# Performance work log

Hardware: AMD Instinct MI355X
Metric: run time of the kernel (lower is better)

The kernel has to match this reference:

```python
import jax, jax.numpy as jnp
import numpy as np

D_MODEL = 1024
N_HEADS = 16
D_K = D_MODEL // N_HEADS
NEG_INF = -1.0e9


def setup_inputs() -> dict:
    key = jax.random.key(0)
    ks = jax.random.split(key, 12)
    B, S = 2, 2048
    inp = {
        "q": jax.random.normal(ks[0], (B, S, D_MODEL), dtype=jnp.float32),
        "k": jax.random.normal(ks[1], (B, S, D_MODEL), dtype=jnp.float32),
        "v": jax.random.normal(ks[2], (B, S, D_MODEL), dtype=jnp.float32),
        "mask": jax.random.randint(ks[3], (B, 1, S, S), 0, 2, dtype=jnp.int32),
        "Wq": jax.random.normal(ks[4], (D_MODEL, D_MODEL), dtype=jnp.float32) / np.sqrt(D_MODEL),
        "bq": jnp.zeros((D_MODEL,), dtype=jnp.float32),
        "Wk": jax.random.normal(ks[5], (D_MODEL, D_MODEL), dtype=jnp.float32) / np.sqrt(D_MODEL),
        "bk": jnp.zeros((D_MODEL,), dtype=jnp.float32),
        "Wv": jax.random.normal(ks[6], (D_MODEL, D_MODEL), dtype=jnp.float32) / np.sqrt(D_MODEL),
        "bv": jnp.zeros((D_MODEL,), dtype=jnp.float32),
        "Wo": jax.random.normal(ks[7], (D_MODEL, D_MODEL), dtype=jnp.float32) / np.sqrt(D_MODEL),
        "bo": jnp.zeros((D_MODEL,), dtype=jnp.float32),
    }
    return inp


def _split_heads(x):
    B, S, _ = x.shape
    return x.reshape(B, S, N_HEADS, D_K).transpose(0, 2, 1, 3)  # [B,H,S,Dk]


def reference(q, k, v, mask, Wq, bq, Wk, bk, Wv, bv, Wo, bo):
    # QKV projections (nn.Linear: x @ W.T + b; here W stored as [in,out]-agnostic square)
    query = _split_heads(q @ Wq + bq)
    key_ = _split_heads(k @ Wk + bk)
    value = _split_heads(v @ Wv + bv)

    scale = 1.0 / np.sqrt(D_K).astype(np.float32)
    scores = jnp.einsum("bhqd,bhkd->bhqk", query, key_) * scale  # [B,H,S,S]
    scores = jnp.where(mask == 0, NEG_INF, scores)
    attn = jax.nn.softmax(scores, axis=-1)  # dropout is identity in eval (p=0.0)
    ctx = jnp.einsum("bhqk,bhkd->bhqd", attn, value)  # [B,H,S,Dk]

    B, H, S, Dk = ctx.shape
    ctx = ctx.transpose(0, 2, 1, 3).reshape(B, S, H * Dk)
    return ctx @ Wo + bo
```

## Files before the change

### kernel.cpp

```cpp
#include <hip/hip_runtime.h>
#include <hip/hip_bf16.h>

typedef __bf16 bf16_t;
typedef __bf16 bf16x2 __attribute__((ext_vector_type(2)));
typedef __bf16 bf16x4 __attribute__((ext_vector_type(4)));
typedef __bf16 bf16x8 __attribute__((ext_vector_type(8)));
typedef float f32x4 __attribute__((ext_vector_type(4)));
typedef float f32x16 __attribute__((ext_vector_type(16)));
typedef int intx4 __attribute__((ext_vector_type(4)));
typedef unsigned int u32;
typedef unsigned long long u64;

#define S_LEN 2048
#define DM 1024
#define NH 16
#define DK 64
#define M_ROWS 4096
#define SCALE_LOG2E 0.1803368801111204f

__device__ __forceinline__ int sw_off(int row, int col) {
  return row * 64 + ((((col >> 3) ^ row) & 7) << 3) + (col & 7);
}

__device__ __forceinline__ bf16x8 cvt8(const float4& a, const float4& b) {
  bf16x8 v;
  v[0] = (__bf16)a.x; v[1] = (__bf16)a.y; v[2] = (__bf16)a.z; v[3] = (__bf16)a.w;
  v[4] = (__bf16)b.x; v[5] = (__bf16)b.y; v[6] = (__bf16)b.z; v[7] = (__bf16)b.w;
  return v;
}

__device__ __forceinline__ void glds16(const bf16_t* g, bf16_t* l) {
  __builtin_amdgcn_global_load_lds(
      (const __attribute__((address_space(1))) void*)g,
      (__attribute__((address_space(3))) void*)l, 16, 0, 0);
}

__device__ __forceinline__ int pk2(float lo, float hi) {
  bf16x2 t;
  t[0] = (__bf16)lo;
  t[1] = (__bf16)hi;
  return __builtin_bit_cast(int, t);
}

__global__ __launch_bounds__(256) void prep(
    const float* __restrict__ q, const float* __restrict__ k,
    const float* __restrict__ v, bf16_t* __restrict__ Xb,
    const float* __restrict__ Wq, const float* __restrict__ Wk,
    const float* __restrict__ Wv, const float* __restrict__ Wo,
    bf16_t* __restrict__ Wt,
    const int* __restrict__ mask, u64* __restrict__ mb)
{
  __shared__ float tile[64][65];
  const int blk = blockIdx.x;
  if (blk < 6144) {
    const int z = blk >> 11;
    const int bx = blk & 2047;
    const float* __restrict__ src = (z == 0) ? q : ((z == 1) ? k : v);
    const size_t idx = ((size_t)bx * 256 + threadIdx.x) * 8;
    const float4 a = *(const float4*)&src[idx];
    const float4 b = *(const float4*)&src[idx + 4];
    *(bf16x8*)&Xb[(size_t)z * M_ROWS * DM + idx] = cvt8(a, b);
  } else if (blk < 7168) {
    const int idx = blk - 6144;
    const int z = idx >> 8, by = (idx >> 4) & 15, bx = idx & 15;
    const float* __restrict__ W = (z == 0) ? Wq : ((z == 1) ? Wk : ((z == 2) ? Wv : Wo));
    bf16_t* __restrict__ out = Wt + (size_t)z * DM * DM;
    const int tx = threadIdx.x & 31, ty = threadIdx.x >> 5;
    const int k0 = bx * 64, n0 = by * 64;
    #pragma unroll
    for (int j = 0; j < 8; ++j) {
      const float2 vv = *(const float2*)&W[(size_t)(k0 + ty + 8 * j) * DM + n0 + tx * 2];
      tile[ty + 8 * j][tx * 2] = vv.x;
      tile[ty + 8 * j][tx * 2 + 1] = vv.y;
    }
    __syncthreads();
    #pragma unroll
    for (int j = 0; j < 8; ++j) {
      const int a = ty + 8 * j;
      bf16x2 p;
      p[0] = (__bf16)tile[tx * 2][a];
      p[1] = (__bf16)tile[tx * 2 + 1][a];
      *(bf16x2*)&out[(size_t)(n0 + a) * DM + k0 + tx * 2] = p;
    }
  } else {
    const int g = (blk - 7168) * 256 + threadIdx.x;
    const int qq = g & 2047;
    const int kw = (g >> 11) & 31;
    const int b = g >> 16;
    const int* src = &mask[((size_t)(b * S_LEN + qq)) * S_LEN + kw * 64];
    u64 bits = 0;
    #pragma unroll
    for (int i = 0; i < 16; ++i) {
      const int4 m4 = *(const int4*)&src[i * 4];
      bits |= (u64)(m4.x != 0) << (4 * i);
      bits |= (u64)(m4.y != 0) << (4 * i + 1);
      bits |= (u64)(m4.z != 0) << (4 * i + 2);
      bits |= (u64)(m4.w != 0) << (4 * i + 3);
    }
    mb[g] = bits;
  }
}

__device__ __forceinline__ void gemm128_body(
    const bf16_t* __restrict__ A, const bf16_t* __restrict__ Bt,
    const float* __restrict__ bias, const float scale,
    bf16_t* __restrict__ outb, float* __restrict__ outf,
    bf16_t* __restrict__ vtw)
{
  __shared__ __align__(16) bf16_t Smem[128 * 136];
  bf16_t* As = Smem;
  bf16_t* Bs = Smem + 4096;
  const int t = threadIdx.x, w = t >> 6, L = t & 63, quad = L >> 4, l16 = L & 15;
  const int m0 = blockIdx.x * 128, n0 = blockIdx.y * 128;
  const int mb = 64 * (w & 1), nb = 64 * (w >> 1);
  const int rowS = t >> 2, subS = (t & 3) * 8;

  f32x4 acc[4][4] = {};
  for (int k0 = 0; k0 < DM; k0 += 32) {
    __syncthreads();
    glds16(&A[(size_t)(m0 + rowS) * DM + k0 + subS],        &As[t * 8]);
    glds16(&A[(size_t)(m0 + 64 + rowS) * DM + k0 + subS],   &As[2048 + t * 8]);
    glds16(&Bt[(size_t)(n0 + rowS) * DM + k0 + subS],       &Bs[t * 8]);
    glds16(&Bt[(size_t)(n0 + 64 + rowS) * DM + k0 + subS],  &Bs[2048 + t * 8]);
    __syncthreads();
    bf16x8 af[4], bfr[4];
    #pragma unroll
    for (int mt = 0; mt < 4; ++mt)
      af[mt] = *(const bf16x8*)&As[(mb + 16 * mt + l16) * 32 + quad * 8];
    #pragma unroll
    for (int ct = 0; ct < 4; ++ct)
      bfr[ct] = *(const bf16x8*)&Bs[(nb + 16 * ct + l16) * 32 + quad * 8];
    #pragma unroll
    for (int mt = 0; mt < 4; ++mt)
      #pragma unroll
      for (int ct = 0; ct < 4; ++ct)
        acc[mt][ct] = __builtin_amdgcn_mfma_f32_16x16x32_bf16(af[mt], bfr[ct], acc[mt][ct], 0, 0, 0);
  }

  if (vtw) {
    __syncthreads();
    #pragma unroll
    for (int mt = 0; mt < 4; ++mt)
      #pragma unroll
      for (int ct = 0; ct < 4; ++ct) {
        const int nloc = nb + 16 * ct + l16;
        const int mloc0 = mb + 16 * mt + quad * 4;
        bf16x4 pk;
        #pragma unroll
        for (int r = 0; r < 4; ++r)
          pk[r] = (__bf16)(acc[mt][ct][r] + bias[n0 + nloc]);
        *(bf16x4*)&Smem[nloc * 136 + mloc0] = pk;
      }
    __syncthreads();
    const int nloc = t >> 1, mh = (t & 1) * 64;
    const int n = n0 + nloc, h = n >> 6, dv = n & 63;
    const int b = m0 >> 11, key0 = (m0 & 2047) + mh;
    bf16_t* dst = &vtw[(((size_t)(b * NH + h)) * DK + dv) * S_LEN + key0];
    #pragma unroll
    for (int j = 0; j < 8; ++j)
      *(bf16x8*)(dst + 8 * j) = *(const bf16x8*)&Smem[nloc * 136 + mh + 8 * j];
    return;
  }

  #pragma unroll
  for (int mt = 0; mt < 4; ++mt)
    #pragma unroll
    for (int ct = 0; ct < 4; ++ct)
      #pragma unroll
      for (int r = 0; r < 4; ++r) {
        const int row = m0 + mb + 16 * mt + quad * 4 + r;
        const int n = n0 + nb + 16 * ct + l16;
        const float val = (acc[mt][ct][r] + bias[n]) * scale;
        if (outb) outb[(size_t)row * DM + n] = (__bf16)val;
        else      outf[(size_t)row * DM + n] = val;
      }
}

__global__ __launch_bounds__(256) void gemm_qkv(
    const bf16_t* __restrict__ Xb, const bf16_t* __restrict__ Wt,
    const float* __restrict__ bq, const float* __restrict__ bk,
    const float* __restrict__ bv, bf16_t* __restrict__ QKVb,
    bf16_t* __restrict__ Vtw)
{
  const int z = blockIdx.z;
  gemm128_body(Xb + (size_t)z * M_ROWS * DM, Wt + (size_t)z * DM * DM,
               (z == 0) ? bq : ((z == 1) ? bk : bv),
               (z == 0) ? SCALE_LOG2E : 1.0f,
               (z == 2) ? nullptr : QKVb + (size_t)z * M_ROWS * DM, nullptr,
               (z == 2) ? Vtw : nullptr);
}

__global__ __launch_bounds__(256) void gemm_out(
    const bf16_t* __restrict__ A, const bf16_t* __restrict__ Bt,
    const float* __restrict__ bias, float* __restrict__ outf)
{
  __shared__ __align__(16) bf16_t As[64 * 32];
  __shared__ __align__(16) bf16_t Bs[128 * 32];
  const int t = threadIdx.x, w = t >> 6, L = t & 63, quad = L >> 4, l16 = L & 15;
  const int m0 = blockIdx.x * 64, n0 = blockIdx.y * 128;
  const int nb = 32 * w;
  const int rowS = t >> 2, subS = (t & 3) * 8;

  f32x4 acc[4][2] = {};
  for (int k0 = 0; k0 < DM; k0 += 32) {
    __syncthreads();
    glds16(&A[(size_t)(m0 + rowS) * DM + k0 + subS],        &As[t * 8]);
    glds16(&Bt[(size_t)(n0 + rowS) * DM + k0 + subS],       &Bs[t * 8]);
    glds16(&Bt[(size_t)(n0 + 64 + rowS) * DM + k0 + subS],  &Bs[2048 + t * 8]);
    __syncthreads();
    bf16x8 af[4], bfr[2];
    #pragma unroll
    for (int mt = 0; mt < 4; ++mt)
      af[mt] = *(const bf16x8*)&As[(16 * mt + l16) * 32 + quad * 8];
    #pragma unroll
    for (int ct = 0; ct < 2; ++ct)
      bfr[ct] = *(const bf16x8*)&Bs[(nb + 16 * ct + l16) * 32 + quad * 8];
    #pragma unroll
    for (int mt = 0; mt < 4; ++mt)
      #pragma unroll
      for (int ct = 0; ct < 2; ++ct)
        acc[mt][ct] = __builtin_amdgcn_mfma_f32_16x16x32_bf16(af[mt], bfr[ct], acc[mt][ct], 0, 0, 0);
  }
  #pragma unroll
  for (int mt = 0; mt < 4; ++mt)
    #pragma unroll
    for (int ct = 0; ct < 2; ++ct)
      #pragma unroll
      for (int r = 0; r < 4; ++r) {
        const int row = m0 + 16 * mt + quad * 4 + r;
        const int n = n0 + nb + 16 * ct + l16;
        outf[(size_t)row * DM + n] = acc[mt][ct][r] + bias[n];
      }
}

__global__ __launch_bounds__(512, 2) void attn_kernel(
    const bf16_t* __restrict__ Qb, const bf16_t* __restrict__ Kb,
    const bf16_t* __restrict__ Vtw, const u64* __restrict__ mb,
    bf16_t* __restrict__ ctx)
{
  __shared__ __align__(16) bf16_t KVs[2][4][64 * 64];

  const int t = threadIdx.x, w = t >> 6, L = t & 63;
  const int l31 = L & 31, h5 = L >> 5;
  const int g = blockIdx.x;
  const int xcd = g & 7, slot = g >> 3;
  const int bh = xcd * 4 + (slot >> 3), qt = slot & 7;
  const int q0 = qt * 256;
  const int b = bh >> 4, h = bh & 15;

  const int qr = q0 + 32 * w + l31;
  bf16x8 qf[4];
  {
    const bf16_t* qsrc = &Qb[(size_t)(b * S_LEN + qr) * DM + h * DK + 8 * h5];
    #pragma unroll
    for (int ks = 0; ks < 4; ++ks) qf[ks] = *(const bf16x8*)(qsrc + 16 * ks);
  }

  const int rk = t >> 3;
  const int ck = (t & 7) ^ (rk & 7);
  const bf16_t* pK = &Kb[(size_t)(b * S_LEN + rk) * DM + h * DK + ck * 8];
  const bf16_t* pV = &Vtw[((size_t)bh * DK + rk) * S_LEN + ck * 8];
  const u64* pm = &mb[(size_t)b * 32 * S_LEN + qr];

  f32x16 O[2] = {};
  float l_lane = 0.f;

  auto compute = [&](const bf16_t* __restrict__ Kc, const bf16_t* __restrict__ Vc,
                     u64 mcur) {
    f32x16 s0 = {}, s1 = {};
    #pragma unroll
    for (int ks = 0; ks < 4; ++ks) {
      const bf16x8 kf0 = *(const bf16x8*)&Kc[sw_off(l31, ks * 16 + 8 * h5)];
      const bf16x8 kf1 = *(const bf16x8*)&Kc[sw_off(32 + l31, ks * 16 + 8 * h5)];
      s0 = __builtin_amdgcn_mfma_f32_32x32x16_bf16(kf0, qf[ks], s0, 0, 0, 0);
      s1 = __builtin_amdgcn_mfma_f32_32x32x16_bf16(kf1, qf[ks], s1, 0, 0, 0);
    }
    #pragma unroll
    for (int nt = 0; nt < 2; ++nt) {
      const u32 mm = ((u32)(mcur >> (nt ? 32 : 0))) >> (4 * h5);
      const f32x16 sacc = nt ? s1 : s0;
      float p[16];
      #pragma unroll
      for (int r = 0; r < 16; ++r) {
        const int cb = (r & 3) + 8 * (r >> 2);
        const u32 mr = (u32)(((int)(mm << (31 - cb))) >> 31);
        const float e = __builtin_exp2f(sacc[r]);
        const float pv = __builtin_bit_cast(float, __builtin_bit_cast(u32, e) & mr);
        l_lane += pv;
        p[r] = pv;
      }
      #pragma unroll
      for (int ss = 0; ss < 2; ++ss) {
        const int x0 = pk2(p[8 * ss + 0], p[8 * ss + 1]);
        const int x1 = pk2(p[8 * ss + 2], p[8 * ss + 3]);
        const int y0 = pk2(p[8 * ss + 4], p[8 * ss + 5]);
        const int y1 = pk2(p[8 * ss + 6], p[8 * ss + 7]);
        const auto r0 = __builtin_amdgcn_permlane32_swap(x0, y0, false, false);
        const auto r1 = __builtin_amdgcn_permlane32_swap(x1, y1, false, false);
        intx4 wv;
        wv[0] = r0[0]; wv[1] = r1[0]; wv[2] = r0[1]; wv[3] = r1[1];
        const bf16x8 pf = __builtin_bit_cast(bf16x8, wv);
        const int s4 = 2 * nt + ss;
        const bf16x8 vf0 = *(const bf16x8*)&Vc[sw_off(l31, s4 * 16 + 8 * h5)];
        const bf16x8 vf1 = *(const bf16x8*)&Vc[sw_off(32 + l31, s4 * 16 + 8 * h5)];
        O[0] = __builtin_amdgcn_mfma_f32_32x32x16_bf16(vf0, pf, O[0], 0, 0, 0);
        O[1] = __builtin_amdgcn_mfma_f32_32x32x16_bf16(vf1, pf, O[1], 0, 0, 0);
      }
    }
  };

  bf16x8 k0r = *(const bf16x8*)pK;
  bf16x8 k1r = *(const bf16x8*)(pK + (size_t)64 * DM);
  bf16x8 v0r = *(const bf16x8*)pV;
  bf16x8 v1r = *(const bf16x8*)(pV + 64);
  u64 m0 = pm[0], m1 = pm[S_LEN];
  pK += (size_t)128 * DM; pV += 128; pm += 2 * S_LEN;
  *(bf16x8*)&KVs[0][0][t * 8] = k0r;
  *(bf16x8*)&KVs[0][1][t * 8] = k1r;
  *(bf16x8*)&KVs[0][2][t * 8] = v0r;
  *(bf16x8*)&KVs[0][3][t * 8] = v1r;
  __syncthreads();

  for (int kt = 0; kt < S_LEN / 128; ++kt) {
    const int cur = kt & 1;
    u64 n0 = 0, n1 = 0;
    if (kt + 1 < S_LEN / 128) {
      k0r = *(const bf16x8*)pK;
      k1r = *(const bf16x8*)(pK + (size_t)64 * DM);
      v0r = *(const bf16x8*)pV;
      v1r = *(const bf16x8*)(pV + 64);
      n0 = pm[0]; n1 = pm[S_LEN];
      pK += (size_t)128 * DM; pV += 128; pm += 2 * S_LEN;
    }
    compute(&KVs[cur][0][0], &KVs[cur][2][0], m0);
    compute(&KVs[cur][1][0], &KVs[cur][3][0], m1);
    if (kt + 1 < S_LEN / 128) {
      *(bf16x8*)&KVs[cur ^ 1][0][t * 8] = k0r;
      *(bf16x8*)&KVs[cur ^ 1][1][t * 8] = k1r;
      *(bf16x8*)&KVs[cur ^ 1][2][t * 8] = v0r;
      *(bf16x8*)&KVs[cur ^ 1][3][t * 8] = v1r;
      m0 = n0; m1 = n1;
    }
    __syncthreads();
  }

  const float lsum = l_lane + __shfl_xor(l_lane, 32);
  const float inv = 1.f / lsum;
  bf16_t* sc = &KVs[0][0][0] + (size_t)w * 2048;
  #pragma unroll
  for (int ot = 0; ot < 2; ++ot)
    #pragma unroll
    for (int r = 0; r < 16; ++r) {
      const int dv = 32 * ot + (r & 3) + 8 * (r >> 2) + 4 * h5;
      sc[sw_off(l31, dv)] = (__bf16)(O[ot][r] * inv);
    }
  const int erow = L >> 1, ecol = (L & 1) * 32;
  bf16_t* dst = &ctx[(size_t)(b * S_LEN + q0 + 32 * w + erow) * DM + h * DK + ecol];
  #pragma unroll
  for (int c8 = 0; c8 < 4; ++c8)
    *(bf16x8*)(dst + 8 * c8) = *(const bf16x8*)&sc[sw_off(erow, ecol + 8 * c8)];
}

extern "C" void kernel_launch(void* const* d_in, const int* in_sizes, int n_in,
                              void* d_out, int out_size, void* d_ws, size_t ws_size,
                              hipStream_t stream) {
  const float* q  = (const float*)d_in[0];
  const float* k  = (const float*)d_in[1];
  const float* v  = (const float*)d_in[2];
  const int* mask = (const int*)d_in[3];
  const float* Wq = (const float*)d_in[4];
  const float* bq = (const float*)d_in[5];
  const float* Wk = (const float*)d_in[6];
  const float* bk = (const float*)d_in[7];
  const float* Wv = (const float*)d_in[8];
  const float* bv = (const float*)d_in[9];
  const float* Wo = (const float*)d_in[10];
  const float* bo = (const float*)d_in[11];
  float* out = (float*)d_out;

  const size_t SLICE = (size_t)M_ROWS * DM;
  bf16_t* Xb   = (bf16_t*)d_ws;
  bf16_t* QKVb = Xb + 3 * SLICE;
  bf16_t* Wt   = QKVb + 3 * SLICE;
  u64* mbw     = (u64*)(Wt + (size_t)4 * DM * DM);
  bf16_t* ctx  = Xb;
  bf16_t* Vtw  = QKVb + 2 * SLICE;

  prep<<<dim3(7680), dim3(256), 0, stream>>>(q, k, v, Xb, Wq, Wk, Wv, Wo, Wt,
                                             mask, mbw);
  gemm_qkv<<<dim3(32, 8, 3), dim3(256), 0, stream>>>(Xb, Wt, bq, bk, bv, QKVb, Vtw);
  attn_kernel<<<dim3(256), dim3(512), 0, stream>>>(QKVb, QKVb + SLICE, Vtw, mbw, ctx);
  gemm_out<<<dim3(64, 8), dim3(256), 0, stream>>>(ctx, Wt + (size_t)3 * DM * DM, bo, out);
}
```

Measured before the change: 281.5 us.

## Fuse prep, QKV GEMM, attention and output GEMM into one cooperative persistent kernel

Replaces the four separate kernel launches with a single cooperative kernel of 256 blocks of 512 threads, using grid.sync between the phases. This removes the launch gaps and inter-kernel drain/fill. In exchange, the GEMM phases now run on only 256 blocks, each handling one 128x128 tile per projection in sequence, where before there were 768 and 512 blocks of 256 threads. The smaller per-wave tile (4x2 MFMAs per k-step) and reduced parallelism may lower GEMM throughput.

```diff
diff --git a/kernel.cpp b/kernel.cpp
--- a/kernel.cpp
+++ b/kernel.cpp
@@ -1,5 +1,8 @@
 #include <hip/hip_runtime.h>
 #include <hip/hip_bf16.h>
+#include <hip/hip_cooperative_groups.h>
+
+namespace cg = cooperative_groups;
 
 typedef __bf16 bf16_t;
 typedef __bf16 bf16x2 __attribute__((ext_vector_type(2)));
@@ -42,323 +45,331 @@
   return __builtin_bit_cast(int, t);
 }
 
-__global__ __launch_bounds__(256) void prep(
+__global__ __launch_bounds__(512, 2) void mega(
     const float* __restrict__ q, const float* __restrict__ k,
-    const float* __restrict__ v, bf16_t* __restrict__ Xb,
-    const float* __restrict__ Wq, const float* __restrict__ Wk,
-    const float* __restrict__ Wv, const float* __restrict__ Wo,
-    bf16_t* __restrict__ Wt,
-    const int* __restrict__ mask, u64* __restrict__ mb)
+    const float* __restrict__ v, const int* __restrict__ mask,
+    const float* __restrict__ Wq, const float* __restrict__ bq,
+    const float* __restrict__ Wk, const float* __restrict__ bk,
+    const float* __restrict__ Wv, const float* __restrict__ bv,
+    const float* __restrict__ Wo, const float* __restrict__ bo,
+    float* __restrict__ out, void* __restrict__ ws)
 {
-  __shared__ float tile[64][65];
-  const int blk = blockIdx.x;
-  if (blk < 6144) {
-    const int z = blk >> 11;
-    const int bx = blk & 2047;
-    const float* __restrict__ src = (z == 0) ? q : ((z == 1) ? k : v);
-    const size_t idx = ((size_t)bx * 256 + threadIdx.x) * 8;
-    const float4 a = *(const float4*)&src[idx];
-    const float4 b = *(const float4*)&src[idx + 4];
-    *(bf16x8*)&Xb[(size_t)z * M_ROWS * DM + idx] = cvt8(a, b);
-  } else if (blk < 7168) {
-    const int idx = blk - 6144;
-    const int z = idx >> 8, by = (idx >> 4) & 15, bx = idx & 15;
-    const float* __restrict__ W = (z == 0) ? Wq : ((z == 1) ? Wk : ((z == 2) ? Wv : Wo));
-    bf16_t* __restrict__ out = Wt + (size_t)z * DM * DM;
-    const int tx = threadIdx.x & 31, ty = threadIdx.x >> 5;
-    const int k0 = bx * 64, n0 = by * 64;
+  __shared__ __align__(16) bf16_t SM[32768];
+
+  const size_t SLICE = (size_t)M_ROWS * DM;
+  bf16_t* Xb   = (bf16_t*)ws;
+  bf16_t* QKVb = Xb + 3 * SLICE;
+  bf16_t* Wt   = QKVb + 3 * SLICE;
+  u64* mbw     = (u64*)(Wt + (size_t)4 * DM * DM);
+  bf16_t* ctx  = Xb;
+  bf16_t* Vtw  = QKVb + 2 * SLICE;
+
+  const int g = blockIdx.x;
+  const int t = threadIdx.x;
+  cg::grid_group grid = cg::this_grid();
+
+  {
+    #pragma unroll 2
+    for (int it = 0; it < 12; ++it) {
+      const int flat = it * 131072 + g * 512 + t;
+      const size_t base = (size_t)flat * 8;
+      const int z = (int)(base >> 22);
+      const size_t off = base & ((size_t)(1u << 22) - 1);
+      const float* __restrict__ src = (z == 0) ? q : ((z == 1) ? k : v);
+      const float4 a = *(const float4*)&src[off];
+      const float4 bb = *(const float4*)&src[off + 4];
+      *(bf16x8*)&Xb[(size_t)z * SLICE + off] = cvt8(a, bb);
+    }
+    {
+      float* tile = (float*)SM;
+      const int half = t >> 8, tt = t & 255;
+      const int tx = tt & 31, ty = tt >> 5;
+      float* myt = tile + half * (64 * 65);
+      for (int it = 0; it < 2; ++it) {
+        __syncthreads();
+        const int tl = g * 4 + it * 2 + half;
+        const int z = tl >> 8, rest = tl & 255, by = rest >> 4, bx = rest & 15;
+        const float* __restrict__ W =
+            (z == 0) ? Wq : ((z == 1) ? Wk : ((z == 2) ? Wv : Wo));
+        bf16_t* __restrict__ outw = Wt + (size_t)z * DM * DM;
+        const int k0 = bx * 64, n0 = by * 64;
+        #pragma unroll
+        for (int j = 0; j < 8; ++j) {
+          const float2 vv =
+              *(const float2*)&W[(size_t)(k0 + ty + 8 * j) * DM + n0 + tx * 2];
+          myt[(ty + 8 * j) * 65 + tx * 2] = vv.x;
+          myt[(ty + 8 * j) * 65 + tx * 2 + 1] = vv.y;
+        }
+        __syncthreads();
+        #pragma unroll
+        for (int j = 0; j < 8; ++j) {
+          const int a = ty + 8 * j;
+          bf16x2 p;
+          p[0] = (__bf16)myt[(tx * 2) * 65 + a];
+          p[1] = (__bf16)myt[(tx * 2 + 1) * 65 + a];
+          *(bf16x2*)&outw[(size_t)(n0 + a) * DM + k0 + tx * 2] = p;
+        }
+      }
+    }
+    {
+      const int gw = g * 512 + t;
+      const int qq = gw & 2047;
+      const int kw = (gw >> 11) & 31;
+      const int b = gw >> 16;
+      const int* src = &mask[((size_t)(b * S_LEN + qq)) * S_LEN + kw * 64];
+      u64 bits = 0;
+      #pragma unroll
+      for (int i = 0; i < 16; ++i) {
+        const int4 m4 = *(const int4*)&src[i * 4];
+        bits |= (u64)(m4.x != 0) << (4 * i);
+        bits |= (u64)(m4.y != 0) << (4 * i + 1);
+        bits |= (u64)(m4.z != 0) << (4 * i + 2);
+        bits |= (u64)(m4.w != 0) << (4 * i + 3);
+      }
+      mbw[gw] = bits;
+    }
+  }
+  grid.sync();
+
+  {
+    bf16_t* As = SM;
+    bf16_t* Bs = SM + 4096;
+    const int w = t >> 6, L = t & 63, quad = L >> 4, l16 = L & 15;
+    const int mb = 64 * (w & 1), nb = 32 * (w >> 1);
+    const int m0 = (g & 31) * 128, n0 = (g >> 5) * 128;
+    const int rowS = t >> 2, subS = (t & 3) * 8;
+    for (int z = 0; z < 3; ++z) {
+      const bf16_t* __restrict__ A = Xb + (size_t)z * SLICE;
+      const bf16_t* __restrict__ Bt = Wt + (size_t)z * DM * DM;
+      const float* __restrict__ bias = (z == 0) ? bq : ((z == 1) ? bk : bv);
+      f32x4 acc[4][2] = {};
+      for (int k0 = 0; k0 < DM; k0 += 32) {
+        __syncthreads();
+        glds16(&A[(size_t)(m0 + rowS) * DM + k0 + subS], &As[t * 8]);
+        glds16(&Bt[(size_t)(n0 + rowS) * DM + k0 + subS], &Bs[t * 8]);
+        __syncthreads();
+        bf16x8 af[4], bfr[2];
+        #pragma unroll
+        for (int mt = 0; mt < 4; ++mt)
+          af[mt] = *(const bf16x8*)&As[(mb + 16 * mt + l16) * 32 + quad * 8];
+        #pragma unroll
+        for (int ct = 0; ct < 2; ++ct)
+          bfr[ct] = *(const bf16x8*)&Bs[(nb + 16 * ct + l16) * 32 + quad * 8];
+        #pragma unroll
+        for (int mt = 0; mt < 4; ++mt)
+          #pragma unroll
+          for (int ct = 0; ct < 2; ++ct)
+            acc[mt][ct] = __builtin_amdgcn_mfma_f32_16x16x32_bf16(
+                af[mt], bfr[ct], acc[mt][ct], 0, 0, 0);
+      }
+      if (z < 2) {
+        const float scale = (z == 0) ? SCALE_LOG2E : 1.0f;
+        bf16_t* __restrict__ outb = QKVb + (size_t)z * SLICE;
+        #pragma unroll
+        for (int mt = 0; mt < 4; ++mt)
+          #pragma unroll
+          for (int ct = 0; ct < 2; ++ct)
+            #pragma unroll
+            for (int r = 0; r < 4; ++r) {
+              const int row = m0 + mb + 16 * mt + quad * 4 + r;
+              const int n = n0 + nb + 16 * ct + l16;
+              outb[(size_t)row * DM + n] =
+                  (__bf16)((acc[mt][ct][r] + bias[n]) * scale);
+            }
+      } else {
+        __syncthreads();
+        bf16_t* Ts = SM;
+        #pragma unroll
+        for (int mt = 0; mt < 4; ++mt)
+          #pragma unroll
+          for (int ct = 0; ct < 2; ++ct) {
+            const int nloc = nb + 16 * ct + l16;
+            const int mloc0 = mb + 16 * mt + quad * 4;
+            bf16x4 pk4;
+            #pragma unroll
+            for (int r = 0; r < 4; ++r)
+              pk4[r] = (__bf16)(acc[mt][ct][r] + bias[n0 + nloc]);
+            *(bf16x4*)&Ts[nloc * 136 + mloc0] = pk4;
+          }
+        __syncthreads();
+        const int nloc = t >> 2, mh = (t & 3) * 32;
+        const int n = n0 + nloc, h = n >> 6, dv = n & 63;
+        const int b = m0 >> 11, key0 = (m0 & 2047) + mh;
+        bf16_t* dst = &Vtw[(((size_t)(b * NH + h)) * DK + dv) * S_LEN + key0];
+        #pragma unroll
+        for (int j = 0; j < 4; ++j)
+          *(bf16x8*)(dst + 8 * j) = *(const bf16x8*)&Ts[nloc * 136 + mh + 8 * j];
+      }
+    }
+  }
+  grid.sync();
+
+  {
+    bf16_t (*KVs)[4][4096] = (bf16_t (*)[4][4096]) & SM[0];
+    const bf16_t* __restrict__ Qb = QKVb;
+    const bf16_t* __restrict__ Kb = QKVb + SLICE;
+    const int w = t >> 6, L = t & 63;
+    const int l31 = L & 31, h5 = L >> 5;
+    const int xcd = g & 7, slot = g >> 3;
+    const int bh = xcd * 4 + (slot >> 3), qt = slot & 7;
+    const int q0 = qt * 256;
+    const int b = bh >> 4, h = bh & 15;
+
+    const int qr = q0 + 32 * w + l31;
+    bf16x8 qf[4];
+    {
+      const bf16_t* qsrc = &Qb[(size_t)(b * S_LEN + qr) * DM + h * DK + 8 * h5];
+      #pragma unroll
+      for (int ks = 0; ks < 4; ++ks) qf[ks] = *(const bf16x8*)(qsrc + 16 * ks);
+    }
+
+    const int rk = t >> 3;
+    const int ck = (t & 7) ^ (rk & 7);
+    const bf16_t* pK = &Kb[(size_t)(b * S_LEN + rk) * DM + h * DK + ck * 8];
+    const bf16_t* pV = &Vtw[((size_t)bh * DK + rk) * S_LEN + ck * 8];
+    const u64* pm = &mbw[(size_t)b * 32 * S_LEN + qr];
+
+    f32x16 O[2] = {};
+    float l_lane = 0.f;
+
+    auto compute = [&](const bf16_t* __restrict__ Kc,
+                       const bf16_t* __restrict__ Vc, u64 mcur) {
+      f32x16 s0 = {}, s1 = {};
+      #pragma unroll
+      for (int ks = 0; ks < 4; ++ks) {
+        const bf16x8 kf0 = *(const bf16x8*)&Kc[sw_off(l31, ks * 16 + 8 * h5)];
+        const bf16x8 kf1 = *(const bf16x8*)&Kc[sw_off(32 + l31, ks * 16 + 8 * h5)];
+        s0 = __builtin_amdgcn_mfma_f32_32x32x16_bf16(kf0, qf[ks], s0, 0, 0, 0);
+        s1 = __builtin_amdgcn_mfma_f32_32x32x16_bf16(kf1, qf[ks], s1, 0, 0, 0);
+      }
+      #pragma unroll
+      for (int nt = 0; nt < 2; ++nt) {
+        const u32 mm = ((u32)(mcur >> (nt ? 32 : 0))) >> (4 * h5);
+        const f32x16 sacc = nt ? s1 : s0;
+        float p[16];
+        #pragma unroll
+        for (int r = 0; r < 16; ++r) {
+          const int cb = (r & 3) + 8 * (r >> 2);
+          const u32 mr = (u32)(((int)(mm << (31 - cb))) >> 31);
+          const float e = __builtin_exp2f(sacc[r]);
+          const float pv = __builtin_bit_cast(float, __builtin_bit_cast(u32, e) & mr);
+          l_lane += pv;
+          p[r] = pv;
+        }
+        #pragma unroll
+        for (int ss = 0; ss < 2; ++ss) {
+          const int x0 = pk2(p[8 * ss + 0], p[8 * ss + 1]);
+          const int x1 = pk2(p[8 * ss + 2], p[8 * ss + 3]);
+          const int y0 = pk2(p[8 * ss + 4], p[8 * ss + 5]);
+          const int y1 = pk2(p[8 * ss + 6], p[8 * ss + 7]);
+          const auto r0 = __builtin_amdgcn_permlane32_swap(x0, y0, false, false);
+          const auto r1 = __builtin_amdgcn_permlane32_swap(x1, y1, false, false);
+          intx4 wv;
+          wv[0] = r0[0]; wv[1] = r1[0]; wv[2] = r0[1]; wv[3] = r1[1];
+          const bf16x8 pf = __builtin_bit_cast(bf16x8, wv);
+          const int s4 = 2 * nt + ss;
+          const bf16x8 vf0 = *(const bf16x8*)&Vc[sw_off(l31, s4 * 16 + 8 * h5)];
+          const bf16x8 vf1 = *(const bf16x8*)&Vc[sw_off(32 + l31, s4 * 16 + 8 * h5)];
+          O[0] = __builtin_amdgcn_mfma_f32_32x32x16_bf16(vf0, pf, O[0], 0, 0, 0);
+          O[1] = __builtin_amdgcn_mfma_f32_32x32x16_bf16(vf1, pf, O[1], 0, 0, 0);
+        }
+      }
+    };
+
+    bf16x8 k0r = *(const bf16x8*)pK;
+    bf16x8 k1r = *(const bf16x8*)(pK + (size_t)64 * DM);
+    bf16x8 v0r = *(const bf16x8*)pV;
+    bf16x8 v1r = *(const bf16x8*)(pV + 64);
+    u64 m0 = pm[0], m1 = pm[S_LEN];
+    pK += (size_t)128 * DM; pV += 128; pm += 2 * S_LEN;
+    *(bf16x8*)&KVs[0][0][t * 8] = k0r;
+    *(bf16x8*)&KVs[0][1][t * 8] = k1r;
+    *(bf16x8*)&KVs[0][2][t * 8] = v0r;
+    *(bf16x8*)&KVs[0][3][t * 8] = v1r;
+    __syncthreads();
+
+    for (int kt = 0; kt < S_LEN / 128; ++kt) {
+      const int cur = kt & 1;
+      u64 n0 = 0, n1 = 0;
+      if (kt + 1 < S_LEN / 128) {
+        k0r = *(const bf16x8*)pK;
+        k1r = *(const bf16x8*)(pK + (size_t)64 * DM);
+        v0r = *(const bf16x8*)pV;
+        v1r = *(const bf16x8*)(pV + 64);
+        n0 = pm[0]; n1 = pm[S_LEN];
+        pK += (size_t)128 * DM; pV += 128; pm += 2 * S_LEN;
+      }
+      compute(&KVs[cur][0][0], &KVs[cur][2][0], m0);
+      compute(&KVs[cur][1][0], &KVs[cur][3][0], m1);
+      if (kt + 1 < S_LEN / 128) {
+        *(bf16x8*)&KVs[cur ^ 1][0][t * 8] = k0r;
+        *(bf16x8*)&KVs[cur ^ 1][1][t * 8] = k1r;
+        *(bf16x8*)&KVs[cur ^ 1][2][t * 8] = v0r;
+        *(bf16x8*)&KVs[cur ^ 1][3][t * 8] = v1r;
+        m0 = n0; m1 = n1;
+      }
+      __syncthreads();
+    }
+
+    const float lsum = l_lane + __shfl_xor(l_lane, 32);
+    const float inv = 1.f / lsum;
+    bf16_t* sc = &SM[0] + (size_t)w * 2048;
     #pragma unroll
-    for (int j = 0; j < 8; ++j) {
-      const float2 vv = *(const float2*)&W[(size_t)(k0 + ty + 8 * j) * DM + n0 + tx * 2];
-      tile[ty + 8 * j][tx * 2] = vv.x;
-      tile[ty + 8 * j][tx * 2 + 1] = vv.y;
-    }
-    __syncthreads();
+    for (int ot = 0; ot < 2; ++ot)
+      #pragma unroll
+      for (int r = 0; r < 16; ++r) {
+        const int dv = 32 * ot + (r & 3) + 8 * (r >> 2) + 4 * h5;
+        sc[sw_off(l31, dv)] = (__bf16)(O[ot][r] * inv);
+      }
+    const int erow = L >> 1, ecol = (L & 1) * 32;
+    bf16_t* dst =
+        &ctx[(size_t)(b * S_LEN + q0 + 32 * w + erow) * DM + h * DK + ecol];
     #pragma unroll
-    for (int j = 0; j < 8; ++j) {
-      const int a = ty + 8 * j;
-      bf16x2 p;
-      p[0] = (__bf16)tile[tx * 2][a];
-      p[1] = (__bf16)tile[tx * 2 + 1][a];
-      *(bf16x2*)&out[(size_t)(n0 + a) * DM + k0 + tx * 2] = p;
-    }
-  } else {
-    const int g = (blk - 7168) * 256 + threadIdx.x;
-    const int qq = g & 2047;
-    const int kw = (g >> 11) & 31;
-    const int b = g >> 16;
-    const int* src = &mask[((size_t)(b * S_LEN + qq)) * S_LEN + kw * 64];
-    u64 bits = 0;
-    #pragma unroll
-    for (int i = 0; i < 16; ++i) {
-      const int4 m4 = *(const int4*)&src[i * 4];
-      bits |= (u64)(m4.x != 0) << (4 * i);
-      bits |= (u64)(m4.y != 0) << (4 * i + 1);
-      bits |= (u64)(m4.z != 0) << (4 * i + 2);
-      bits |= (u64)(m4.w != 0) << (4 * i + 3);
-    }
-    mb[g] = bits;
+    for (int c8 = 0; c8 < 4; ++c8)
+      *(bf16x8*)(dst + 8 * c8) = *(const bf16x8*)&sc[sw_off(erow, ecol + 8 * c8)];
   }
-}
-
-__device__ __forceinline__ void gemm128_body(
-    const bf16_t* __restrict__ A, const bf16_t* __restrict__ Bt,
-    const float* __restrict__ bias, const float scale,
-    bf16_t* __restrict__ outb, float* __restrict__ outf,
-    bf16_t* __restrict__ vtw)
-{
-  __shared__ __align__(16) bf16_t Smem[128 * 136];
-  bf16_t* As = Smem;
-  bf16_t* Bs = Smem + 4096;
-  const int t = threadIdx.x, w = t >> 6, L = t & 63, quad = L >> 4, l16 = L & 15;
-  const int m0 = blockIdx.x * 128, n0 = blockIdx.y * 128;
-  const int mb = 64 * (w & 1), nb = 64 * (w >> 1);
-  const int rowS = t >> 2, subS = (t & 3) * 8;
-
-  f32x4 acc[4][4] = {};
-  for (int k0 = 0; k0 < DM; k0 += 32) {
-    __syncthreads();
-    glds16(&A[(size_t)(m0 + rowS) * DM + k0 + subS],        &As[t * 8]);
-    glds16(&A[(size_t)(m0 + 64 + rowS) * DM + k0 + subS],   &As[2048 + t * 8]);
-    glds16(&Bt[(size_t)(n0 + rowS) * DM + k0 + subS],       &Bs[t * 8]);
-    glds16(&Bt[(size_t)(n0 + 64 + rowS) * DM + k0 + subS],  &Bs[2048 + t * 8]);
-    __syncthreads();
-    bf16x8 af[4], bfr[4];
+  grid.sync();
+
+  {
+    bf16_t* As = SM;
+    bf16_t* Bs = SM + 4096;
+    const bf16_t* __restrict__ A = ctx;
+    const bf16_t* __restrict__ Bt = Wt + (size_t)3 * DM * DM;
+    const int w = t >> 6, L = t & 63, quad = L >> 4, l16 = L & 15;
+    const int mb = 64 * (w & 1), nb = 32 * (w >> 1);
+    const int m0 = (g & 31) * 128, n0 = (g >> 5) * 128;
+    const int rowS = t >> 2, subS = (t & 3) * 8;
+    f32x4 acc[4][2] = {};
+    for (int k0 = 0; k0 < DM; k0 += 32) {
+      __syncthreads();
+      glds16(&A[(size_t)(m0 + rowS) * DM + k0 + subS], &As[t * 8]);
+      glds16(&Bt[(size_t)(n0 + rowS) * DM + k0 + subS], &Bs[t * 8]);
+      __syncthreads();
+      bf16x8 af[4], bfr[2];
+      #pragma unroll
+      for (int mt = 0; mt < 4; ++mt)
+        af[mt] = *(const bf16x8*)&As[(mb + 16 * mt + l16) * 32 + quad * 8];
+      #pragma unroll
+      for (int ct = 0; ct < 2; ++ct)
+        bfr[ct] = *(const bf16x8*)&Bs[(nb + 16 * ct + l16) * 32 + quad * 8];
+      #pragma unroll
+      for (int mt = 0; mt < 4; ++mt)
+        #pragma unroll
+        for (int ct = 0; ct < 2; ++ct)
+          acc[mt][ct] = __builtin_amdgcn_mfma_f32_16x16x32_bf16(
+              af[mt], bfr[ct], acc[mt][ct], 0, 0, 0);
+    }
     #pragma unroll
     for (int mt = 0; mt < 4; ++mt)
-      af[mt] = *(const bf16x8*)&As[(mb + 16 * mt + l16) * 32 + quad * 8];
-    #pragma unroll
-    for (int ct = 0; ct < 4; ++ct)
-      bfr[ct] = *(const bf16x8*)&Bs[(nb + 16 * ct + l16) * 32 + quad * 8];
-    #pragma unroll
-    for (int mt = 0; mt < 4; ++mt)
-      #pragma unroll
-      for (int ct = 0; ct < 4; ++ct)
-        acc[mt][ct] = __builtin_amdgcn_mfma_f32_16x16x32_bf16(af[mt], bfr[ct], acc[mt][ct], 0, 0, 0);
+      #pragma unroll
+      for (int ct = 0; ct < 2; ++ct)
+        #pragma unroll
+        for (int r = 0; r < 4; ++r) {
+          const int row = m0 + mb + 16 * mt + quad * 4 + r;
+          const int n = n0 + nb + 16 * ct + l16;
+          out[(size_t)row * DM + n] = acc[mt][ct][r] + bo[n];
+        }
   }
-
-  if (vtw) {
-    __syncthreads();
-    #pragma unroll
-    for (int mt = 0; mt < 4; ++mt)
-      #pragma unroll
-      for (int ct = 0; ct < 4; ++ct) {
-        const int nloc = nb + 16 * ct + l16;
-        const int mloc0 = mb + 16 * mt + quad * 4;
-        bf16x4 pk;
-        #pragma unroll
-        for (int r = 0; r < 4; ++r)
-          pk[r] = (__bf16)(acc[mt][ct][r] + bias[n0 + nloc]);
-        *(bf16x4*)&Smem[nloc * 136 + mloc0] = pk;
-      }
-    __syncthreads();
-    const int nloc = t >> 1, mh = (t & 1) * 64;
-    const int n = n0 + nloc, h = n >> 6, dv = n & 63;
-    const int b = m0 >> 11, key0 = (m0 & 2047) + mh;
-    bf16_t* dst = &vtw[(((size_t)(b * NH + h)) * DK + dv) * S_LEN + key0];
-    #pragma unroll
-    for (int j = 0; j < 8; ++j)
-      *(bf16x8*)(dst + 8 * j) = *(const bf16x8*)&Smem[nloc * 136 + mh + 8 * j];
-    return;
-  }
-
-  #pragma unroll
-  for (int mt = 0; mt < 4; ++mt)
-    #pragma unroll
-    for (int ct = 0; ct < 4; ++ct)
-      #pragma unroll
-      for (int r = 0; r < 4; ++r) {
-        const int row = m0 + mb + 16 * mt + quad * 4 + r;
-        const int n = n0 + nb + 16 * ct + l16;
-        const float val = (acc[mt][ct][r] + bias[n]) * scale;
-        if (outb) outb[(size_t)row * DM + n] = (__bf16)val;
-        else      outf[(size_t)row * DM + n] = val;
-      }
-}
-
-__global__ __launch_bounds__(256) void gemm_qkv(
-    const bf16_t* __restrict__ Xb, const bf16_t* __restrict__ Wt,
-    const float* __restrict__ bq, const float* __restrict__ bk,
-    const float* __restrict__ bv, bf16_t* __restrict__ QKVb,
-    bf16_t* __restrict__ Vtw)
-{
-  const int z = blockIdx.z;
-  gemm128_body(Xb + (size_t)z * M_ROWS * DM, Wt + (size_t)z * DM * DM,
-               (z == 0) ? bq : ((z == 1) ? bk : bv),
-               (z == 0) ? SCALE_LOG2E : 1.0f,
-               (z == 2) ? nullptr : QKVb + (size_t)z * M_ROWS * DM, nullptr,
-               (z == 2) ? Vtw : nullptr);
-}
-
-__global__ __launch_bounds__(256) void gemm_out(
-    const bf16_t* __restrict__ A, const bf16_t* __restrict__ Bt,
-    const float* __restrict__ bias, float* __restrict__ outf)
-{
-  __shared__ __align__(16) bf16_t As[64 * 32];
-  __shared__ __align__(16) bf16_t Bs[128 * 32];
-  const int t = threadIdx.x, w = t >> 6, L = t & 63, quad = L >> 4, l16 = L & 15;
-  const int m0 = blockIdx.x * 64, n0 = blockIdx.y * 128;
-  const int nb = 32 * w;
-  const int rowS = t >> 2, subS = (t & 3) * 8;
-
-  f32x4 acc[4][2] = {};
-  for (int k0 = 0; k0 < DM; k0 += 32) {
-    __syncthreads();
-    glds16(&A[(size_t)(m0 + rowS) * DM + k0 + subS],        &As[t * 8]);
-    glds16(&Bt[(size_t)(n0 + rowS) * DM + k0 + subS],       &Bs[t * 8]);
-    glds16(&Bt[(size_t)(n0 + 64 + rowS) * DM + k0 + subS],  &Bs[2048 + t * 8]);
-    __syncthreads();
-    bf16x8 af[4], bfr[2];
-    #pragma unroll
-    for (int mt = 0; mt < 4; ++mt)
-      af[mt] = *(const bf16x8*)&As[(16 * mt + l16) * 32 + quad * 8];
-    #pragma unroll
-    for (int ct = 0; ct < 2; ++ct)
-      bfr[ct] = *(const bf16x8*)&Bs[(nb + 16 * ct + l16) * 32 + quad * 8];
-    #pragma unroll
-    for (int mt = 0; mt < 4; ++mt)
-      #pragma unroll
-      for (int ct = 0; ct < 2; ++ct)
-        acc[mt][ct] = __builtin_amdgcn_mfma_f32_16x16x32_bf16(af[mt], bfr[ct], acc[mt][ct], 0, 0, 0);
-  }
-  #pragma unroll
-  for (int mt = 0; mt < 4; ++mt)
-    #pragma unroll
-    for (int ct = 0; ct < 2; ++ct)
-      #pragma unroll
-      for (int r = 0; r < 4; ++r) {
-        const int row = m0 + 16 * mt + quad * 4 + r;
-        const int n = n0 + nb + 16 * ct + l16;
-        outf[(size_t)row * DM + n] = acc[mt][ct][r] + bias[n];
-      }
-}
-
-__global__ __launch_bounds__(512, 2) void attn_kernel(
-    const bf16_t* __restrict__ Qb, const bf16_t* __restrict__ Kb,
-    const bf16_t* __restrict__ Vtw, const u64* __restrict__ mb,
-    bf16_t* __restrict__ ctx)
-{
-  __shared__ __align__(16) bf16_t KVs[2][4][64 * 64];
-
-  const int t = threadIdx.x, w = t >> 6, L = t & 63;
-  const int l31 = L & 31, h5 = L >> 5;
-  const int g = blockIdx.x;
-  const int xcd = g & 7, slot = g >> 3;
-  const int bh = xcd * 4 + (slot >> 3), qt = slot & 7;
-  const int q0 = qt * 256;
-  const int b = bh >> 4, h = bh & 15;
-
-  const int qr = q0 + 32 * w + l31;
-  bf16x8 qf[4];
-  {
-    const bf16_t* qsrc = &Qb[(size_t)(b * S_LEN + qr) * DM + h * DK + 8 * h5];
-    #pragma unroll
-    for (int ks = 0; ks < 4; ++ks) qf[ks] = *(const bf16x8*)(qsrc + 16 * ks);
-  }
-
-  const int rk = t >> 3;
-  const int ck = (t & 7) ^ (rk & 7);
-  const bf16_t* pK = &Kb[(size_t)(b * S_LEN + rk) * DM + h * DK + ck * 8];
-  const bf16_t* pV = &Vtw[((size_t)bh * DK + rk) * S_LEN + ck * 8];
-  const u64* pm = &mb[(size_t)b * 32 * S_LEN + qr];
-
-  f32x16 O[2] = {};
-  float l_lane = 0.f;
-
-  auto compute = [&](const bf16_t* __restrict__ Kc, const bf16_t* __restrict__ Vc,
-                     u64 mcur) {
-    f32x16 s0 = {}, s1 = {};
-    #pragma unroll
-    for (int ks = 0; ks < 4; ++ks) {
-      const bf16x8 kf0 = *(const bf16x8*)&Kc[sw_off(l31, ks * 16 + 8 * h5)];
-      const bf16x8 kf1 = *(const bf16x8*)&Kc[sw_off(32 + l31, ks * 16 + 8 * h5)];
-      s0 = __builtin_amdgcn_mfma_f32_32x32x16_bf16(kf0, qf[ks], s0, 0, 0, 0);
-      s1 = __builtin_amdgcn_mfma_f32_32x32x16_bf16(kf1, qf[ks], s1, 0, 0, 0);
-    }
-    #pragma unroll
-    for (int nt = 0; nt < 2; ++nt) {
-      const u32 mm = ((u32)(mcur >> (nt ? 32 : 0))) >> (4 * h5);
-      const f32x16 sacc = nt ? s1 : s0;
-      float p[16];
-      #pragma unroll
-      for (int r = 0; r < 16; ++r) {
-        const int cb = (r & 3) + 8 * (r >> 2);
-        const u32 mr = (u32)(((int)(mm << (31 - cb))) >> 31);
-        const float e = __builtin_exp2f(sacc[r]);
-        const float pv = __builtin_bit_cast(float, __builtin_bit_cast(u32, e) & mr);
-        l_lane += pv;
-        p[r] = pv;
-      }
-      #pragma unroll
-      for (int ss = 0; ss < 2; ++ss) {
-        const int x0 = pk2(p[8 * ss + 0], p[8 * ss + 1]);
-        const int x1 = pk2(p[8 * ss + 2], p[8 * ss + 3]);
-        const int y0 = pk2(p[8 * ss + 4], p[8 * ss + 5]);
-        const int y1 = pk2(p[8 * ss + 6], p[8 * ss + 7]);
-        const auto r0 = __builtin_amdgcn_permlane32_swap(x0, y0, false, false);
-        const auto r1 = __builtin_amdgcn_permlane32_swap(x1, y1, false, false);
-        intx4 wv;
-        wv[0] = r0[0]; wv[1] = r1[0]; wv[2] = r0[1]; wv[3] = r1[1];
-        const bf16x8 pf = __builtin_bit_cast(bf16x8, wv);
-        const int s4 = 2 * nt + ss;
-        const bf16x8 vf0 = *(const bf16x8*)&Vc[sw_off(l31, s4 * 16 + 8 * h5)];
-        const bf16x8 vf1 = *(const bf16x8*)&Vc[sw_off(32 + l31, s4 * 16 + 8 * h5)];
-        O[0] = __builtin_amdgcn_mfma_f32_32x32x16_bf16(vf0, pf, O[0], 0, 0, 0);
-        O[1] = __builtin_amdgcn_mfma_f32_32x32x16_bf16(vf1, pf, O[1], 0, 0, 0);
-      }
-    }
-  };
-
-  bf16x8 k0r = *(const bf16x8*)pK;
-  bf16x8 k1r = *(const bf16x8*)(pK + (size_t)64 * DM);
-  bf16x8 v0r = *(const bf16x8*)pV;
-  bf16x8 v1r = *(const bf16x8*)(pV + 64);
-  u64 m0 = pm[0], m1 = pm[S_LEN];
-  pK += (size_t)128 * DM; pV += 128; pm += 2 * S_LEN;
-  *(bf16x8*)&KVs[0][0][t * 8] = k0r;
-  *(bf16x8*)&KVs[0][1][t * 8] = k1r;
-  *(bf16x8*)&KVs[0][2][t * 8] = v0r;
-  *(bf16x8*)&KVs[0][3][t * 8] = v1r;
-  __syncthreads();
-
-  for (int kt = 0; kt < S_LEN / 128; ++kt) {
-    const int cur = kt & 1;
-    u64 n0 = 0, n1 = 0;
-    if (kt + 1 < S_LEN / 128) {
-      k0r = *(const bf16x8*)pK;
-      k1r = *(const bf16x8*)(pK + (size_t)64 * DM);
-      v0r = *(const bf16x8*)pV;
-      v1r = *(const bf16x8*)(pV + 64);
-      n0 = pm[0]; n1 = pm[S_LEN];
-      pK += (size_t)128 * DM; pV += 128; pm += 2 * S_LEN;
-    }
-    compute(&KVs[cur][0][0], &KVs[cur][2][0], m0);
-    compute(&KVs[cur][1][0], &KVs[cur][3][0], m1);
-    if (kt + 1 < S_LEN / 128) {
-      *(bf16x8*)&KVs[cur ^ 1][0][t * 8] = k0r;
-      *(bf16x8*)&KVs[cur ^ 1][1][t * 8] = k1r;
-      *(bf16x8*)&KVs[cur ^ 1][2][t * 8] = v0r;
-      *(bf16x8*)&KVs[cur ^ 1][3][t * 8] = v1r;
-      m0 = n0; m1 = n1;
-    }
-    __syncthreads();
-  }
-
-  const float lsum = l_lane + __shfl_xor(l_lane, 32);
-  const float inv = 1.f / lsum;
-  bf16_t* sc = &KVs[0][0][0] + (size_t)w * 2048;
-  #pragma unroll
-  for (int ot = 0; ot < 2; ++ot)
-    #pragma unroll
-    for (int r = 0; r < 16; ++r) {
-      const int dv = 32 * ot + (r & 3) + 8 * (r >> 2) + 4 * h5;
-      sc[sw_off(l31, dv)] = (__bf16)(O[ot][r] * inv);
-    }
-  const int erow = L >> 1, ecol = (L & 1) * 32;
-  bf16_t* dst = &ctx[(size_t)(b * S_LEN + q0 + 32 * w + erow) * DM + h * DK + ecol];
-  #pragma unroll
-  for (int c8 = 0; c8 < 4; ++c8)
-    *(bf16x8*)(dst + 8 * c8) = *(const bf16x8*)&sc[sw_off(erow, ecol + 8 * c8)];
 }
 
 extern "C" void kernel_launch(void* const* d_in, const int* in_sizes, int n_in,
@@ -377,18 +388,12 @@
   const float* Wo = (const float*)d_in[10];
   const float* bo = (const float*)d_in[11];
   float* out = (float*)d_out;
-
-  const size_t SLICE = (size_t)M_ROWS * DM;
-  bf16_t* Xb   = (bf16_t*)d_ws;
-  bf16_t* QKVb = Xb + 3 * SLICE;
-  bf16_t* Wt   = QKVb + 3 * SLICE;
-  u64* mbw     = (u64*)(Wt + (size_t)4 * DM * DM);
-  bf16_t* ctx  = Xb;
-  bf16_t* Vtw  = QKVb + 2 * SLICE;
-
-  prep<<<dim3(7680), dim3(256), 0, stream>>>(q, k, v, Xb, Wq, Wk, Wv, Wo, Wt,
-                                             mask, mbw);
-  gemm_qkv<<<dim3(32, 8, 3), dim3(256), 0, stream>>>(Xb, Wt, bq, bk, bv, QKVb, Vtw);
-  attn_kernel<<<dim3(256), dim3(512), 0, stream>>>(QKVb, QKVb + SLICE, Vtw, mbw, ctx);
-  gemm_out<<<dim3(64, 8), dim3(256), 0, stream>>>(ctx, Wt + (size_t)3 * DM * DM, bo, out);
-}
+  void* ws = d_ws;
+
+  void* args[] = {
+      (void*)&q,  (void*)&k,  (void*)&v,  (void*)&mask,
+      (void*)&Wq, (void*)&bq, (void*)&Wk, (void*)&bk,
+      (void*)&Wv, (void*)&bv, (void*)&Wo, (void*)&bo,
+      (void*)&out, (void*)&ws};
+  hipLaunchCooperativeKernel((void*)mega, dim3(256), dim3(512), args, 0, stream);
+}
```

After: 422.4 us. +50.1%, slower.
